# Kernel optimization log

Measured on AMD Instinct MI355X. Metric: run time of the kernel, lower is better.

## Reference

```python
import jax, jax.numpy as jnp
import numpy as np

N_LAYERS = 3

def setup_inputs() -> dict:
    key = jax.random.key(0)
    ks = jax.random.split(key, 16)
    N, E, F_in, H = 50000, 800000, 5, 64
    x = jax.random.normal(ks[0], (N, F_in), dtype=jnp.float32)
    edge_index = jax.random.randint(ks[1], (2, E), 0, N, dtype=jnp.int64)
    s = lambda fan_in: 1.0 / np.sqrt(fan_in)
    return {
        "x": x,
        "edge_index": edge_index,
        "W_enc": jax.random.uniform(ks[2], (F_in, H), jnp.float32, -s(F_in), s(F_in)),
        "b_enc": jnp.zeros((H,), jnp.float32),
        "conv_W": jax.random.uniform(ks[3], (N_LAYERS, H, H), jnp.float32, -s(H), s(H)),
        "conv_b": jnp.zeros((N_LAYERS, H), jnp.float32),
        "W_d1": jax.random.uniform(ks[4], (H, H // 2), jnp.float32, -s(H), s(H)),
        "b_d1": jnp.zeros((H // 2,), jnp.float32),
        "W_d2": jax.random.uniform(ks[5], (H // 2, 1), jnp.float32, -s(H // 2), s(H // 2)),
        "b_d2": jnp.zeros((1,), jnp.float32),
        "W_i1": jax.random.uniform(ks[6], (H, H // 2), jnp.float32, -s(H), s(H)),
        "b_i1": jnp.zeros((H // 2,), jnp.float32),
        "W_i2": jax.random.uniform(ks[7], (H // 2, 1), jnp.float32, -s(H // 2), s(H // 2)),
        "b_i2": jnp.zeros((1,), jnp.float32),
    }

def reference(x, edge_index, W_enc, b_enc, conv_W, conv_b,
              W_d1, b_d1, W_d2, b_d2, W_i1, b_i1, W_i2, b_i2):
    N = x.shape[0]
    # GCN normalization with self-loops (PyG GCNConv default):
    loops = jnp.arange(N, dtype=edge_index.dtype)
    row = jnp.concatenate([edge_index[0], loops])  # source
    col = jnp.concatenate([edge_index[1], loops])  # target
    deg = jax.ops.segment_sum(jnp.ones_like(row, dtype=x.dtype), col, num_segments=N)
    dinv = jax.lax.rsqrt(deg)  # deg >= 1 due to self-loops
    norm = dinv[row] * dinv[col]  # [E + N]

    h = jax.nn.relu(x @ W_enc + b_enc)  # [N, H]
    for l in range(N_LAYERS):
        hw = h @ conv_W[l]                       # [N, H]
        msg = hw[row] * norm[:, None]            # gather + scale
        agg = jax.ops.segment_sum(msg, col, num_segments=N)  # scatter-add
        h = jax.nn.relu(agg + conv_b[l])

    demand = jax.nn.relu(h @ W_d1 + b_d1) @ W_d2 + b_d2       # [N, 1]
    inventory = jax.nn.relu(h @ W_i1 + b_i1) @ W_i2 + b_i2    # [N, 1]
    return (demand, inventory)
```

## Files before the change

kernel.cpp:

```cpp
#include <hip/hip_runtime.h>
#include <hip/hip_bf16.h>


#define HDIM 64
#define PB 256
#define NPB 256
#define NPB_SHIFT 8

__device__ inline unsigned bfpack(float lo, float hi) {
    unsigned ul = __float_as_uint(lo), uh = __float_as_uint(hi);
    ul += 0x7fffu + ((ul >> 16) & 1u);
    uh += 0x7fffu + ((uh >> 16) & 1u);
    return (ul >> 16) | (uh & 0xffff0000u);
}

__device__ inline float2 bfunpack(unsigned u) {
    float2 r;
    r.x = __uint_as_float(u << 16);
    r.y = __uint_as_float(u & 0xffff0000u);
    return r;
}

__global__ __launch_bounds__(256) void hist_pass(const int* __restrict__ dst,
                                                 unsigned* __restrict__ histT,
                                                 int E, int NB) {
    __shared__ unsigned h[256];
    int t = threadIdx.x, p = blockIdx.x;
    h[t] = 0u;
    __syncthreads();
    int chunk = (E + PB - 1) / PB;
    int lo = p * chunk, hi = min(lo + chunk, E);
    for (int e = lo + t; e < hi; e += 256)
        atomicAdd(&h[dst[e] >> NPB_SHIFT], 1u);
    __syncthreads();
    if (t < NB) histT[t * PB + p] = h[t];
}

__global__ __launch_bounds__(PB) void scan_bucket(unsigned* __restrict__ histT,
                                                  unsigned* __restrict__ btot) {
    __shared__ unsigned s[PB];
    int t = threadIdx.x, k = blockIdx.x;
    unsigned v = histT[k * PB + t];
    s[t] = v;
    __syncthreads();
#pragma unroll
    for (int off = 1; off < PB; off <<= 1) {
        unsigned u = (t >= off) ? s[t - off] : 0u;
        __syncthreads();
        s[t] += u;
        __syncthreads();
    }
    histT[k * PB + t] = s[t] - v;
    if (t == PB - 1) btot[k] = s[t];
}

__global__ __launch_bounds__(256) void bin_pass(const int* __restrict__ ei,
                                                const unsigned* __restrict__ histT,
                                                const unsigned* __restrict__ btot,
                                                unsigned* __restrict__ ebuf,
                                                int E, int NB) {
    __shared__ unsigned bb[256];
    __shared__ unsigned cur[256];
    int t = threadIdx.x, p = blockIdx.x;
    unsigned bv = (t < NB) ? btot[t] : 0u;
    bb[t] = bv;
    __syncthreads();
#pragma unroll
    for (int off = 1; off < 256; off <<= 1) {
        unsigned u = (t >= off) ? bb[t - off] : 0u;
        __syncthreads();
        bb[t] += u;
        __syncthreads();
    }
    if (t < NB) cur[t] = histT[t * PB + p] + (bb[t] - bv);
    __syncthreads();
    int chunk = (E + PB - 1) / PB;
    int lo = p * chunk, hi = min(lo + chunk, E);
    for (int e = lo + t; e < hi; e += 256) {
        unsigned sN = (unsigned)ei[e];
        unsigned dN = (unsigned)ei[E + e];
        unsigned pos = atomicAdd(&cur[dN >> NPB_SHIFT], 1u);
        ebuf[pos] = ((dN & (NPB - 1u)) << 16) | sN;
    }
}

__global__ __launch_bounds__(256) void csr_pass(const unsigned* __restrict__ ebuf,
                                                const unsigned* __restrict__ btot,
                                                unsigned* __restrict__ row_ptr,
                                                float* __restrict__ dinv,
                                                int* __restrict__ csr_src,
                                                int N, int E, int NB) {
    __shared__ unsigned bb[256];
    __shared__ unsigned cntL[NPB];
    __shared__ unsigned sc[NPB];
    __shared__ unsigned cur[NPB];
    int t = threadIdx.x, k = blockIdx.x;
    unsigned bv = (t < NB) ? btot[t] : 0u;
    bb[t] = bv;
    __syncthreads();
#pragma unroll
    for (int off = 1; off < 256; off <<= 1) {
        unsigned u = (t >= off) ? bb[t - off] : 0u;
        __syncthreads();
        bb[t] += u;
        __syncthreads();
    }
    unsigned e1 = bb[k];
    unsigned e0 = e1 - btot[k];
    int nbase = k << NPB_SHIFT;
    cntL[t] = 0u;
    __syncthreads();
    for (unsigned e = e0 + t; e < e1; e += 256)
        atomicAdd(&cntL[ebuf[e] >> 16], 1u);
    __syncthreads();
    unsigned v = cntL[t];
    sc[t] = v;
    __syncthreads();
#pragma unroll
    for (int off = 1; off < NPB; off <<= 1) {
        unsigned u = (t >= off) ? sc[t - off] : 0u;
        __syncthreads();
        sc[t] += u;
        __syncthreads();
    }
    unsigned pos0 = e0 + sc[t] - v;
    cur[t] = pos0;
    int node = nbase + t;
    if (node < N) {
        row_ptr[node] = pos0;
        dinv[node] = rsqrtf((float)(v + 1u));
    }
    if (k == NB - 1 && t == 0) row_ptr[N] = (unsigned)E;
    __syncthreads();
    for (unsigned e = e0 + t; e < e1; e += 256) {
        unsigned ed = ebuf[e];
        unsigned pos = atomicAdd(&cur[ed >> 16], 1u);
        csr_src[pos] = (int)(ed & 0xffffu);
    }
}

__global__ __launch_bounds__(256) void encoder(const float* __restrict__ x,
                                               const float* __restrict__ W,
                                               const float* __restrict__ b,
                                               const float* __restrict__ dinv,
                                               unsigned* __restrict__ hn, int N) {
    int t = blockIdx.x * 256 + threadIdx.x;
    int i = t >> 5, jp = t & 31;
    if (i >= N) return;
    int j0 = 2 * jp;
    float a0 = b[j0], a1 = b[j0 + 1];
#pragma unroll
    for (int k = 0; k < 5; k++) {
        float xv = x[i * 5 + k];
        a0 = fmaf(xv, W[k * 64 + j0], a0);
        a1 = fmaf(xv, W[k * 64 + j0 + 1], a1);
    }
    float di = dinv[i];
    hn[t] = bfpack(di * fmaxf(a0, 0.0f), di * fmaxf(a1, 0.0f));
}

#define ACC4(A, V) do {                                                         \
    float2 _p = bfunpack((V).x), _q = bfunpack((V).y);                          \
    (A).x += _p.x; (A).y += _p.y; (A).z += _q.x; (A).w += _q.y;                 \
} while (0)

#define MACC4(A, V, C) do {                                                     \
    float2 _p = bfunpack((V).x), _q = bfunpack((V).y);                          \
    (A).x += (C) ? _p.x : 0.f; (A).y += (C) ? _p.y : 0.f;                       \
    (A).z += (C) ? _q.x : 0.f; (A).w += (C) ? _q.y : 0.f;                       \
} while (0)

__device__ inline float4 gather_row_q(const unsigned* __restrict__ row_ptr,
                                      const int* __restrict__ csr_src,
                                      const uint2* __restrict__ hp,
                                      int i, int fl) {
    uint2 sv = hp[(size_t)i * 16 + fl];
    float4 a0, a1 = {0.f, 0.f, 0.f, 0.f}, a2 = a1, a3 = a1;
    {
        float2 p = bfunpack(sv.x), q = bfunpack(sv.y);
        a0.x = p.x; a0.y = p.y; a0.z = q.x; a0.w = q.y;
    }
    unsigned e0 = row_ptr[i];
    unsigned cnt = row_ptr[i + 1] - e0;
    const int* idx = csr_src + e0;
    unsigned u = 0;
    if (cnt >= 8) {
        int s0 = idx[0], s1 = idx[1], s2 = idx[2], s3 = idx[3];
        int s4 = idx[4], s5 = idx[5], s6 = idx[6], s7 = idx[7];
        while (true) {
            uint2 v0 = hp[(size_t)s0 * 16 + fl];
            uint2 v1 = hp[(size_t)s1 * 16 + fl];
            uint2 v2 = hp[(size_t)s2 * 16 + fl];
            uint2 v3 = hp[(size_t)s3 * 16 + fl];
            uint2 v4 = hp[(size_t)s4 * 16 + fl];
            uint2 v5 = hp[(size_t)s5 * 16 + fl];
            uint2 v6 = hp[(size_t)s6 * 16 + fl];
            uint2 v7 = hp[(size_t)s7 * 16 + fl];
            unsigned un = u + 8;
            bool more = (un + 8 <= cnt);
            if (more) {
                s0 = idx[un + 0]; s1 = idx[un + 1]; s2 = idx[un + 2]; s3 = idx[un + 3];
                s4 = idx[un + 4]; s5 = idx[un + 5]; s6 = idx[un + 6]; s7 = idx[un + 7];
            }
            ACC4(a0, v0); ACC4(a1, v1); ACC4(a2, v2); ACC4(a3, v3);
            ACC4(a0, v4); ACC4(a1, v5); ACC4(a2, v6); ACC4(a3, v7);
            u = un;
            if (!more) break;
        }
    }
    if (u < cnt) {
        unsigned last = cnt - 1;
        int t0 = idx[u];
        int t1 = idx[min(u + 1, last)];
        int t2 = idx[min(u + 2, last)];
        int t3 = idx[min(u + 3, last)];
        int t4 = idx[min(u + 4, last)];
        int t5 = idx[min(u + 5, last)];
        int t6 = idx[min(u + 6, last)];
        int t7 = idx[min(u + 7, last)];
        uint2 w0 = hp[(size_t)t0 * 16 + fl];
        uint2 w1 = hp[(size_t)t1 * 16 + fl];
        uint2 w2 = hp[(size_t)t2 * 16 + fl];
        uint2 w3 = hp[(size_t)t3 * 16 + fl];
        uint2 w4 = hp[(size_t)t4 * 16 + fl];
        uint2 w5 = hp[(size_t)t5 * 16 + fl];
        uint2 w6 = hp[(size_t)t6 * 16 + fl];
        uint2 w7 = hp[(size_t)t7 * 16 + fl];
        ACC4(a0, w0);
        MACC4(a1, w1, u + 1 < cnt);
        MACC4(a2, w2, u + 2 < cnt);
        MACC4(a3, w3, u + 3 < cnt);
        MACC4(a0, w4, u + 4 < cnt);
        MACC4(a1, w5, u + 5 < cnt);
        MACC4(a2, w6, u + 6 < cnt);
        MACC4(a3, w7, u + 7 < cnt);
    }
    a0.x += a1.x; a0.y += a1.y; a0.z += a1.z; a0.w += a1.w;
    a2.x += a3.x; a2.y += a3.y; a2.z += a3.z; a2.w += a3.w;
    a0.x += a2.x; a0.y += a2.y; a0.z += a2.z; a0.w += a2.w;
    return a0;
}

#define CONV_K8(WROW, HK) do {                                                  \
    float4 wa = ((const float4*)(WROW))[0];                                     \
    float4 wb = ((const float4*)(WROW))[1];                                     \
    acc0.x = fmaf(HK, wa.x, acc0.x); acc0.y = fmaf(HK, wa.y, acc0.y);           \
    acc0.z = fmaf(HK, wa.z, acc0.z); acc0.w = fmaf(HK, wa.w, acc0.w);           \
    acc1.x = fmaf(HK, wb.x, acc1.x); acc1.y = fmaf(HK, wb.y, acc1.y);           \
    acc1.z = fmaf(HK, wb.z, acc1.z); acc1.w = fmaf(HK, wb.w, acc1.w);           \
} while (0)

__global__ __launch_bounds__(512, 6) void gconv(const unsigned* __restrict__ row_ptr,
                                                const int* __restrict__ csr_src,
                                                const unsigned* __restrict__ hn_in,
                                                const float* __restrict__ W,
                                                const float* __restrict__ b,
                                                const float* __restrict__ dinv,
                                                unsigned* __restrict__ hn_out, int N) {
    __shared__ float ybuf[64 * 65];
    int tid = threadIdx.x;
    int qw = tid >> 4, fl = tid & 15;
    int base = blockIdx.x * 64;
    for (int s = 0; s < 2; s++) {
        int n = qw * 2 + s;
        int i = base + n;
        if (i < N) {
            float4 a = gather_row_q(row_ptr, csr_src, (const uint2*)hn_in, i, fl);
            ybuf[(4 * fl + 0) * 65 + n] = a.x;
            ybuf[(4 * fl + 1) * 65 + n] = a.y;
            ybuf[(4 * fl + 2) * 65 + n] = a.z;
            ybuf[(4 * fl + 3) * 65 + n] = a.w;
        }
    }
    __syncthreads();
    int n = tid & 63;
    int qt = __builtin_amdgcn_readfirstlane(tid >> 6);
    int i = base + n;
    if (i >= N) return;
    int jb = qt * 8;
    float di = dinv[i];
    float4 acc0 = {0.f, 0.f, 0.f, 0.f}, acc1 = acc0;
    const float* Wj = W + jb;
#pragma unroll
    for (int k = 0; k < 64; k++) {
        float hk = ybuf[k * 65 + n];
        CONV_K8(Wj + k * 64, hk);
    }
    const float* bj = b + jb;
    float4 y0, y1;
    y0.x = fmaxf(fmaf(di, acc0.x, bj[0]), 0.f) * di;
    y0.y = fmaxf(fmaf(di, acc0.y, bj[1]), 0.f) * di;
    y0.z = fmaxf(fmaf(di, acc0.z, bj[2]), 0.f) * di;
    y0.w = fmaxf(fmaf(di, acc0.w, bj[3]), 0.f) * di;
    y1.x = fmaxf(fmaf(di, acc1.x, bj[4]), 0.f) * di;
    y1.y = fmaxf(fmaf(di, acc1.y, bj[5]), 0.f) * di;
    y1.z = fmaxf(fmaf(di, acc1.z, bj[6]), 0.f) * di;
    y1.w = fmaxf(fmaf(di, acc1.w, bj[7]), 0.f) * di;
    uint4 p;
    p.x = bfpack(y0.x, y0.y);
    p.y = bfpack(y0.z, y0.w);
    p.z = bfpack(y1.x, y1.y);
    p.w = bfpack(y1.z, y1.w);
    *(uint4*)(hn_out + (size_t)i * 32 + qt * 4) = p;
}

__global__ __launch_bounds__(512, 6) void gconv_heads(const unsigned* __restrict__ row_ptr,
                                                      const int* __restrict__ csr_src,
                                                      const unsigned* __restrict__ hn_in,
                                                      const float* __restrict__ W,
                                                      const float* __restrict__ b,
                                                      const float* __restrict__ dinv,
                                                      const float* __restrict__ W_d1, const float* __restrict__ b_d1,
                                                      const float* __restrict__ W_d2, const float* __restrict__ b_d2,
                                                      const float* __restrict__ W_i1, const float* __restrict__ b_i1,
                                                      const float* __restrict__ W_i2, const float* __restrict__ b_i2,
                                                      float* __restrict__ out, int N) {
    __shared__ float ybuf[64 * 65];
    __shared__ float opart[512];
    int tid = threadIdx.x;
    int qw = tid >> 4, fl = tid & 15;
    int base = blockIdx.x * 64;
    for (int s = 0; s < 2; s++) {
        int n = qw * 2 + s;
        int i = base + n;
        if (i < N) {
            float4 a = gather_row_q(row_ptr, csr_src, (const uint2*)hn_in, i, fl);
            ybuf[(4 * fl + 0) * 65 + n] = a.x;
            ybuf[(4 * fl + 1) * 65 + n] = a.y;
            ybuf[(4 * fl + 2) * 65 + n] = a.z;
            ybuf[(4 * fl + 3) * 65 + n] = a.w;
        }
    }
    __syncthreads();
    int n = tid & 63;
    int qt = __builtin_amdgcn_readfirstlane(tid >> 6);
    int i = base + n;
    int jb = qt * 8;
    float y[8];
    if (i < N) {
        float di = dinv[i];
        float4 acc0 = {0.f, 0.f, 0.f, 0.f}, acc1 = acc0;
        const float* Wj = W + jb;
#pragma unroll
        for (int k = 0; k < 64; k++) {
            float hk = ybuf[k * 65 + n];
            CONV_K8(Wj + k * 64, hk);
        }
        const float* bj = b + jb;
        y[0] = fmaxf(fmaf(di, acc0.x, bj[0]), 0.f);
        y[1] = fmaxf(fmaf(di, acc0.y, bj[1]), 0.f);
        y[2] = fmaxf(fmaf(di, acc0.z, bj[2]), 0.f);
        y[3] = fmaxf(fmaf(di, acc0.w, bj[3]), 0.f);
        y[4] = fmaxf(fmaf(di, acc1.x, bj[4]), 0.f);
        y[5] = fmaxf(fmaf(di, acc1.y, bj[5]), 0.f);
        y[6] = fmaxf(fmaf(di, acc1.z, bj[6]), 0.f);
        y[7] = fmaxf(fmaf(di, acc1.w, bj[7]), 0.f);
    }
    __syncthreads();
    if (i < N) {
#pragma unroll
        for (int jj = 0; jj < 8; jj++) ybuf[(jb + jj) * 65 + n] = y[jj];
    }
    __syncthreads();
    int hd = __builtin_amdgcn_readfirstlane(tid >> 8);
    int q2 = __builtin_amdgcn_readfirstlane((tid >> 6) & 3);
    int hb = q2 * 8;
    float op = 0.f;
    if (i < N) {
        const float* W1 = (hd ? W_i1 : W_d1) + hb;
        const float* b1 = (hd ? b_i1 : b_d1) + hb;
        const float* W2 = (hd ? W_i2 : W_d2) + hb;
        float4 acc0 = {0.f, 0.f, 0.f, 0.f}, acc1 = acc0;
#pragma unroll
        for (int k = 0; k < 64; k++) {
            float hk = ybuf[k * 65 + n];
            CONV_K8(W1 + k * 32, hk);
        }
        op = fmaf(fmaxf(acc0.x + b1[0], 0.f), W2[0], op);
        op = fmaf(fmaxf(acc0.y + b1[1], 0.f), W2[1], op);
        op = fmaf(fmaxf(acc0.z + b1[2], 0.f), W2[2], op);
        op = fmaf(fmaxf(acc0.w + b1[3], 0.f), W2[3], op);
        op = fmaf(fmaxf(acc1.x + b1[4], 0.f), W2[4], op);
        op = fmaf(fmaxf(acc1.y + b1[5], 0.f), W2[5], op);
        op = fmaf(fmaxf(acc1.z + b1[6], 0.f), W2[6], op);
        op = fmaf(fmaxf(acc1.w + b1[7], 0.f), W2[7], op);
    }
    opart[tid] = op;
    __syncthreads();
    if (tid < 128) {
        int n2 = tid & 63, h2 = tid >> 6;
        int i2 = base + n2;
        if (i2 < N) {
            int o0 = h2 * 256 + n2;
            float o = opart[o0] + opart[o0 + 64] + opart[o0 + 128] + opart[o0 + 192]
                    + (h2 ? b_i2[0] : b_d2[0]);
            out[(size_t)h2 * N + i2] = o;
        }
    }
}

extern "C" void kernel_launch(void* const* d_in, const int* in_sizes, int n_in,
                              void* d_out, int out_size, void* d_ws, size_t ws_size,
                              hipStream_t stream) {
    const float* x      = (const float*)d_in[0];
    const int*   ei     = (const int*)d_in[1];
    const float* W_enc  = (const float*)d_in[2];
    const float* b_enc  = (const float*)d_in[3];
    const float* conv_W = (const float*)d_in[4];
    const float* conv_b = (const float*)d_in[5];
    const float* W_d1   = (const float*)d_in[6];
    const float* b_d1   = (const float*)d_in[7];
    const float* W_d2   = (const float*)d_in[8];
    const float* b_d2   = (const float*)d_in[9];
    const float* W_i1   = (const float*)d_in[10];
    const float* b_i1   = (const float*)d_in[11];
    const float* W_i2   = (const float*)d_in[12];
    const float* b_i2   = (const float*)d_in[13];

    const int N = in_sizes[0] / 5;
    const int E = in_sizes[1] / 2;
    const int NB = (N + NPB - 1) >> NPB_SHIFT;

    float* g    = (float*)d_ws;
    unsigned* hnA = (unsigned*)d_ws;
    unsigned* hnB = (unsigned*)(g + (size_t)N * HDIM);
    float* dinv = (float*)(hnB + (size_t)N * 32);
    unsigned* row_ptr = (unsigned*)(dinv + N);
    unsigned* histT   = row_ptr + N + 1;
    unsigned* btot    = histT + (size_t)NB * PB;
    int* csr_src      = (int*)(btot + NB);
    unsigned* ebuf    = (unsigned*)d_ws;
    float* out = (float*)d_out;

    const int gBlocks = (N + 63) / 64;

    hist_pass<<<PB, 256, 0, stream>>>(ei + E, histT, E, NB);
    scan_bucket<<<NB, PB, 0, stream>>>(histT, btot);
    bin_pass<<<PB, 256, 0, stream>>>(ei, histT, btot, ebuf, E, NB);
    csr_pass<<<NB, 256, 0, stream>>>(ebuf, btot, row_ptr, dinv, csr_src, N, E, NB);

    encoder<<<(N * 32 + 255) / 256, 256, 0, stream>>>(x, W_enc, b_enc, dinv, hnA, N);

    gconv<<<gBlocks, 512, 0, stream>>>(row_ptr, csr_src, hnA,
                                       conv_W + 0 * HDIM * HDIM, conv_b + 0 * HDIM,
                                       dinv, hnB, N);
    gconv<<<gBlocks, 512, 0, stream>>>(row_ptr, csr_src, hnB,
                                       conv_W + 1 * HDIM * HDIM, conv_b + 1 * HDIM,
                                       dinv, hnA, N);
    gconv_heads<<<gBlocks, 512, 0, stream>>>(row_ptr, csr_src, hnA,
                                             conv_W + 2 * HDIM * HDIM, conv_b + 2 * HDIM,
                                             dinv, W_d1, b_d1, W_d2, b_d2,
                                             W_i1, b_i1, W_i2, b_i2, out, N);
}
```

Measured before the change: 223.2 us.

## Split neighbor gather by source half into two passes for cache locality

Partitions each node's CSR neighbor list by whether the source index is below a fixed midpoint (NHALF). Each layer then runs two kernels: a first pass gathers from the low half and writes fp32 partial sums to a scratch buffer, and a second pass gathers from the high half, adds the partial, and does the dense transform. The aim is to keep each pass's randomly gathered working set small enough to stay resident in cache. The cost is an extra kernel launch per layer plus writing and reading a fp32 N×64 partial buffer. Nontemporal loads and stores are used so this streaming traffic does not evict the gathered data.

Measured after the change: 263.2 us. 17.9% more time.

```diff
diff --git a/kernel.cpp b/kernel.cpp
--- a/kernel.cpp
+++ b/kernel.cpp
@@ -6,6 +6,7 @@
 #define PB 256
 #define NPB 256
 #define NPB_SHIFT 8
+#define NHALF 25000
 
 __device__ inline unsigned bfpack(float lo, float hi) {
     unsigned ul = __float_as_uint(lo), uh = __float_as_uint(hi);
@@ -19,6 +20,27 @@
     r.x = __uint_as_float(u << 16);
     r.y = __uint_as_float(u & 0xffff0000u);
     return r;
+}
+
+__device__ inline void nt_store4(float* p, float4 v) {
+    __builtin_nontemporal_store(v.x, p + 0);
+    __builtin_nontemporal_store(v.y, p + 1);
+    __builtin_nontemporal_store(v.z, p + 2);
+    __builtin_nontemporal_store(v.w, p + 3);
+}
+__device__ inline float4 nt_load4(const float* p) {
+    float4 v;
+    v.x = __builtin_nontemporal_load(p + 0);
+    v.y = __builtin_nontemporal_load(p + 1);
+    v.z = __builtin_nontemporal_load(p + 2);
+    v.w = __builtin_nontemporal_load(p + 3);
+    return v;
+}
+__device__ inline void nt_store4u(unsigned* p, uint4 v) {
+    __builtin_nontemporal_store(v.x, p + 0);
+    __builtin_nontemporal_store(v.y, p + 1);
+    __builtin_nontemporal_store(v.z, p + 2);
+    __builtin_nontemporal_store(v.w, p + 3);
 }
 
 __global__ __launch_bounds__(256) void hist_pass(const int* __restrict__ dst,
@@ -87,13 +109,16 @@
 __global__ __launch_bounds__(256) void csr_pass(const unsigned* __restrict__ ebuf,
                                                 const unsigned* __restrict__ btot,
                                                 unsigned* __restrict__ row_ptr,
+                                                unsigned* __restrict__ midp,
                                                 float* __restrict__ dinv,
                                                 int* __restrict__ csr_src,
                                                 int N, int E, int NB) {
     __shared__ unsigned bb[256];
     __shared__ unsigned cntL[NPB];
+    __shared__ unsigned cnt0[NPB];
     __shared__ unsigned sc[NPB];
-    __shared__ unsigned cur[NPB];
+    __shared__ unsigned curA[NPB];
+    __shared__ unsigned curB[NPB];
     int t = threadIdx.x, k = blockIdx.x;
     unsigned bv = (t < NB) ? btot[t] : 0u;
     bb[t] = bv;
@@ -109,9 +134,14 @@
     unsigned e0 = e1 - btot[k];
     int nbase = k << NPB_SHIFT;
     cntL[t] = 0u;
-    __syncthreads();
-    for (unsigned e = e0 + t; e < e1; e += 256)
-        atomicAdd(&cntL[ebuf[e] >> 16], 1u);
+    cnt0[t] = 0u;
+    __syncthreads();
+    for (unsigned e = e0 + t; e < e1; e += 256) {
+        unsigned ed = ebuf[e];
+        unsigned local = ed >> 16;
+        atomicAdd(&cntL[local], 1u);
+        if ((ed & 0xffffu) < NHALF) atomicAdd(&cnt0[local], 1u);
+    }
     __syncthreads();
     unsigned v = cntL[t];
     sc[t] = v;
@@ -124,18 +154,23 @@
         __syncthreads();
     }
     unsigned pos0 = e0 + sc[t] - v;
-    cur[t] = pos0;
+    curA[t] = pos0;
+    curB[t] = pos0 + cnt0[t];
     int node = nbase + t;
     if (node < N) {
         row_ptr[node] = pos0;
+        midp[node] = pos0 + cnt0[t];
         dinv[node] = rsqrtf((float)(v + 1u));
     }
     if (k == NB - 1 && t == 0) row_ptr[N] = (unsigned)E;
     __syncthreads();
     for (unsigned e = e0 + t; e < e1; e += 256) {
         unsigned ed = ebuf[e];
-        unsigned pos = atomicAdd(&cur[ed >> 16], 1u);
-        csr_src[pos] = (int)(ed & 0xffffu);
+        unsigned local = ed >> 16;
+        unsigned src = ed & 0xffffu;
+        unsigned pos = (src < NHALF) ? atomicAdd(&curA[local], 1u)
+                                     : atomicAdd(&curB[local], 1u);
+        csr_src[pos] = (int)src;
     }
 }
 
@@ -170,19 +205,10 @@
     (A).z += (C) ? _q.x : 0.f; (A).w += (C) ? _q.y : 0.f;                       \
 } while (0)
 
-__device__ inline float4 gather_row_q(const unsigned* __restrict__ row_ptr,
-                                      const int* __restrict__ csr_src,
-                                      const uint2* __restrict__ hp,
-                                      int i, int fl) {
-    uint2 sv = hp[(size_t)i * 16 + fl];
-    float4 a0, a1 = {0.f, 0.f, 0.f, 0.f}, a2 = a1, a3 = a1;
-    {
-        float2 p = bfunpack(sv.x), q = bfunpack(sv.y);
-        a0.x = p.x; a0.y = p.y; a0.z = q.x; a0.w = q.y;
-    }
-    unsigned e0 = row_ptr[i];
-    unsigned cnt = row_ptr[i + 1] - e0;
-    const int* idx = csr_src + e0;
+__device__ inline float4 gather_range_q(const int* __restrict__ idx, unsigned cnt,
+                                        const uint2* __restrict__ hp, int fl,
+                                        float4 a0) {
+    float4 a1 = {0.f, 0.f, 0.f, 0.f}, a2 = a1, a3 = a1;
     unsigned u = 0;
     if (cnt >= 8) {
         int s0 = idx[0], s1 = idx[1], s2 = idx[2], s3 = idx[3];
@@ -241,6 +267,33 @@
     return a0;
 }
 
+__global__ __launch_bounds__(512, 6) void gpart(const unsigned* __restrict__ row_ptr,
+                                                const unsigned* __restrict__ midp,
+                                                const int* __restrict__ csr_src,
+                                                const unsigned* __restrict__ hn_in,
+                                                float* __restrict__ g, int N) {
+    int tid = threadIdx.x;
+    int qw = tid >> 4, fl = tid & 15;
+    int base = blockIdx.x * 64;
+    const uint2* hp = (const uint2*)hn_in;
+    for (int s = 0; s < 2; s++) {
+        int n = qw * 2 + s;
+        int i = base + n;
+        if (i < N) {
+            unsigned e0 = row_ptr[i];
+            unsigned e1 = midp[i];
+            float4 a = {0.f, 0.f, 0.f, 0.f};
+            if (i < NHALF) {
+                uint2 sv = hp[(size_t)i * 16 + fl];
+                float2 p = bfunpack(sv.x), q = bfunpack(sv.y);
+                a.x = p.x; a.y = p.y; a.z = q.x; a.w = q.y;
+            }
+            a = gather_range_q(csr_src + e0, e1 - e0, hp, fl, a);
+            nt_store4(g + (size_t)i * 64 + 4 * fl, a);
+        }
+    }
+}
+
 #define CONV_K8(WROW, HK) do {                                                  \
     float4 wa = ((const float4*)(WROW))[0];                                     \
     float4 wb = ((const float4*)(WROW))[1];                                     \
@@ -250,22 +303,35 @@
     acc1.z = fmaf(HK, wb.z, acc1.z); acc1.w = fmaf(HK, wb.w, acc1.w);           \
 } while (0)
 
-__global__ __launch_bounds__(512, 6) void gconv(const unsigned* __restrict__ row_ptr,
-                                                const int* __restrict__ csr_src,
-                                                const unsigned* __restrict__ hn_in,
-                                                const float* __restrict__ W,
-                                                const float* __restrict__ b,
-                                                const float* __restrict__ dinv,
-                                                unsigned* __restrict__ hn_out, int N) {
+__global__ __launch_bounds__(512, 6) void gconvB(const unsigned* __restrict__ row_ptr,
+                                                 const unsigned* __restrict__ midp,
+                                                 const int* __restrict__ csr_src,
+                                                 const unsigned* __restrict__ hn_in,
+                                                 const float* __restrict__ g,
+                                                 const float* __restrict__ W,
+                                                 const float* __restrict__ b,
+                                                 const float* __restrict__ dinv,
+                                                 unsigned* __restrict__ hn_out, int N) {
     __shared__ float ybuf[64 * 65];
     int tid = threadIdx.x;
     int qw = tid >> 4, fl = tid & 15;
     int base = blockIdx.x * 64;
+    const uint2* hp = (const uint2*)hn_in;
     for (int s = 0; s < 2; s++) {
         int n = qw * 2 + s;
         int i = base + n;
         if (i < N) {
-            float4 a = gather_row_q(row_ptr, csr_src, (const uint2*)hn_in, i, fl);
+            unsigned e0 = midp[i];
+            unsigned e1 = row_ptr[i + 1];
+            float4 a = {0.f, 0.f, 0.f, 0.f};
+            if (i >= NHALF) {
+                uint2 sv = hp[(size_t)i * 16 + fl];
+                float2 p = bfunpack(sv.x), q = bfunpack(sv.y);
+                a.x = p.x; a.y = p.y; a.z = q.x; a.w = q.y;
+            }
+            a = gather_range_q(csr_src + e0, e1 - e0, hp, fl, a);
+            float4 part = nt_load4(g + (size_t)i * 64 + 4 * fl);
+            a.x += part.x; a.y += part.y; a.z += part.z; a.w += part.w;
             ybuf[(4 * fl + 0) * 65 + n] = a.x;
             ybuf[(4 * fl + 1) * 65 + n] = a.y;
             ybuf[(4 * fl + 2) * 65 + n] = a.z;
@@ -301,30 +367,43 @@
     p.y = bfpack(y0.z, y0.w);
     p.z = bfpack(y1.x, y1.y);
     p.w = bfpack(y1.z, y1.w);
-    *(uint4*)(hn_out + (size_t)i * 32 + qt * 4) = p;
-}
-
-__global__ __launch_bounds__(512, 6) void gconv_heads(const unsigned* __restrict__ row_ptr,
-                                                      const int* __restrict__ csr_src,
-                                                      const unsigned* __restrict__ hn_in,
-                                                      const float* __restrict__ W,
-                                                      const float* __restrict__ b,
-                                                      const float* __restrict__ dinv,
-                                                      const float* __restrict__ W_d1, const float* __restrict__ b_d1,
-                                                      const float* __restrict__ W_d2, const float* __restrict__ b_d2,
-                                                      const float* __restrict__ W_i1, const float* __restrict__ b_i1,
-                                                      const float* __restrict__ W_i2, const float* __restrict__ b_i2,
-                                                      float* __restrict__ out, int N) {
+    nt_store4u(hn_out + (size_t)i * 32 + qt * 4, p);
+}
+
+__global__ __launch_bounds__(512, 6) void gconvB_heads(const unsigned* __restrict__ row_ptr,
+                                                       const unsigned* __restrict__ midp,
+                                                       const int* __restrict__ csr_src,
+                                                       const unsigned* __restrict__ hn_in,
+                                                       const float* __restrict__ g,
+                                                       const float* __restrict__ W,
+                                                       const float* __restrict__ b,
+                                                       const float* __restrict__ dinv,
+                                                       const float* __restrict__ W_d1, const float* __restrict__ b_d1,
+                                                       const float* __restrict__ W_d2, const float* __restrict__ b_d2,
+                                                       const float* __restrict__ W_i1, const float* __restrict__ b_i1,
+                                                       const float* __restrict__ W_i2, const float* __restrict__ b_i2,
+                                                       float* __restrict__ out, int N) {
     __shared__ float ybuf[64 * 65];
     __shared__ float opart[512];
     int tid = threadIdx.x;
     int qw = tid >> 4, fl = tid & 15;
     int base = blockIdx.x * 64;
+    const uint2* hp = (const uint2*)hn_in;
     for (int s = 0; s < 2; s++) {
         int n = qw * 2 + s;
         int i = base + n;
         if (i < N) {
-            float4 a = gather_row_q(row_ptr, csr_src, (const uint2*)hn_in, i, fl);
+            unsigned e0 = midp[i];
+            unsigned e1 = row_ptr[i + 1];
+            float4 a = {0.f, 0.f, 0.f, 0.f};
+            if (i >= NHALF) {
+                uint2 sv = hp[(size_t)i * 16 + fl];
+                float2 p = bfunpack(sv.x), q = bfunpack(sv.y);
+                a.x = p.x; a.y = p.y; a.z = q.x; a.w = q.y;
+            }
+            a = gather_range_q(csr_src + e0, e1 - e0, hp, fl, a);
+            float4 part = nt_load4(g + (size_t)i * 64 + 4 * fl);
+            a.x += part.x; a.y += part.y; a.z += part.z; a.w += part.w;
             ybuf[(4 * fl + 0) * 65 + n] = a.x;
             ybuf[(4 * fl + 1) * 65 + n] = a.y;
             ybuf[(4 * fl + 2) * 65 + n] = a.z;
@@ -422,11 +501,12 @@
     const int NB = (N + NPB - 1) >> NPB_SHIFT;
 
     float* g    = (float*)d_ws;
-    unsigned* hnA = (unsigned*)d_ws;
-    unsigned* hnB = (unsigned*)(g + (size_t)N * HDIM);
+    unsigned* hnA = (unsigned*)(g + (size_t)N * HDIM);
+    unsigned* hnB = hnA + (size_t)N * 32;
     float* dinv = (float*)(hnB + (size_t)N * 32);
     unsigned* row_ptr = (unsigned*)(dinv + N);
-    unsigned* histT   = row_ptr + N + 1;
+    unsigned* midp    = row_ptr + N + 1;
+    unsigned* histT   = midp + N;
     unsigned* btot    = histT + (size_t)NB * PB;
     int* csr_src      = (int*)(btot + NB);
     unsigned* ebuf    = (unsigned*)d_ws;
@@ -437,18 +517,21 @@
     hist_pass<<<PB, 256, 0, stream>>>(ei + E, histT, E, NB);
     scan_bucket<<<NB, PB, 0, stream>>>(histT, btot);
     bin_pass<<<PB, 256, 0, stream>>>(ei, histT, btot, ebuf, E, NB);
-    csr_pass<<<NB, 256, 0, stream>>>(ebuf, btot, row_ptr, dinv, csr_src, N, E, NB);
+    csr_pass<<<NB, 256, 0, stream>>>(ebuf, btot, row_ptr, midp, dinv, csr_src, N, E, NB);
 
     encoder<<<(N * 32 + 255) / 256, 256, 0, stream>>>(x, W_enc, b_enc, dinv, hnA, N);
 
-    gconv<<<gBlocks, 512, 0, stream>>>(row_ptr, csr_src, hnA,
-                                       conv_W + 0 * HDIM * HDIM, conv_b + 0 * HDIM,
-                                       dinv, hnB, N);
-    gconv<<<gBlocks, 512, 0, stream>>>(row_ptr, csr_src, hnB,
-                                       conv_W + 1 * HDIM * HDIM, conv_b + 1 * HDIM,
-                                       dinv, hnA, N);
-    gconv_heads<<<gBlocks, 512, 0, stream>>>(row_ptr, csr_src, hnA,
-                                             conv_W + 2 * HDIM * HDIM, conv_b + 2 * HDIM,
-                                             dinv, W_d1, b_d1, W_d2, b_d2,
-                                             W_i1, b_i1, W_i2, b_i2, out, N);
-}
+    gpart<<<gBlocks, 512, 0, stream>>>(row_ptr, midp, csr_src, hnA, g, N);
+    gconvB<<<gBlocks, 512, 0, stream>>>(row_ptr, midp, csr_src, hnA, g,
+                                        conv_W + 0 * HDIM * HDIM, conv_b + 0 * HDIM,
+                                        dinv, hnB, N);
+    gpart<<<gBlocks, 512, 0, stream>>>(row_ptr, midp, csr_src, hnB, g, N);
+    gconvB<<<gBlocks, 512, 0, stream>>>(row_ptr, midp, csr_src, hnB, g,
+                                        conv_W + 1 * HDIM * HDIM, conv_b + 1 * HDIM,
+                                        dinv, hnA, N);
+    gpart<<<gBlocks, 512, 0, stream>>>(row_ptr, midp, csr_src, hnA, g, N);
+    gconvB_heads<<<gBlocks, 512, 0, stream>>>(row_ptr, midp, csr_src, hnA, g,
+                                              conv_W + 2 * HDIM * HDIM, conv_b + 2 * HDIM,
+                                              dinv, W_d1, b_d1, W_d2, b_d2,
+                                              W_i1, b_i1, W_i2, b_i2, out, N);
+}
```

## Pad CSR neighbor lists to multiples of eight with a zero sentinel row

Applied to the files above, without the earlier changes.

Each node's neighbor list is padded to a multiple of 8 inside fixed-capacity per-bucket slabs, with pad entries pointing at an extra zero feature row N. The gather loop then drops its masked tail iteration and the row_ptr[i+1] read, and uses a per-node count of 8-blocks stored as uint16. Padding adds wasted gathers of the zero row (on average about 3.5 per node). The fixed BCAP=8192 slab per bucket assumes no bucket holds more than that many padded edges. Launch bounds occupancy hint is lowered from 6 to 4.

Measured after the change: 207.2 us (median of 2 runs). 1.08x faster.

```diff
diff --git a/kernel.cpp b/kernel.cpp
--- a/kernel.cpp
+++ b/kernel.cpp
@@ -6,6 +6,7 @@
 #define PB 256
 #define NPB 256
 #define NPB_SHIFT 8
+#define BCAP 8192
 
 __device__ inline unsigned bfpack(float lo, float hi) {
     unsigned ul = __float_as_uint(lo), uh = __float_as_uint(hi);
@@ -87,8 +88,9 @@
 __global__ __launch_bounds__(256) void csr_pass(const unsigned* __restrict__ ebuf,
                                                 const unsigned* __restrict__ btot,
                                                 unsigned* __restrict__ row_ptr,
+                                                unsigned short* __restrict__ pc8,
                                                 float* __restrict__ dinv,
-                                                int* __restrict__ csr_src,
+                                                int* __restrict__ csr_pad,
                                                 int N, int E, int NB) {
     __shared__ unsigned bb[256];
     __shared__ unsigned cntL[NPB];
@@ -114,7 +116,8 @@
         atomicAdd(&cntL[ebuf[e] >> 16], 1u);
     __syncthreads();
     unsigned v = cntL[t];
-    sc[t] = v;
+    unsigned pcnt = (v + 7u) & ~7u;
+    sc[t] = pcnt;
     __syncthreads();
 #pragma unroll
     for (int off = 1; off < NPB; off <<= 1) {
@@ -123,19 +126,20 @@
         sc[t] += u;
         __syncthreads();
     }
-    unsigned pos0 = e0 + sc[t] - v;
+    unsigned pos0 = (unsigned)k * BCAP + (sc[t] - pcnt);
     cur[t] = pos0;
     int node = nbase + t;
     if (node < N) {
         row_ptr[node] = pos0;
+        pc8[node] = (unsigned short)(pcnt >> 3);
         dinv[node] = rsqrtf((float)(v + 1u));
-    }
-    if (k == NB - 1 && t == 0) row_ptr[N] = (unsigned)E;
+        for (unsigned j = v; j < pcnt; j++) csr_pad[pos0 + j] = N;
+    }
     __syncthreads();
     for (unsigned e = e0 + t; e < e1; e += 256) {
         unsigned ed = ebuf[e];
         unsigned pos = atomicAdd(&cur[ed >> 16], 1u);
-        csr_src[pos] = (int)(ed & 0xffffu);
+        csr_pad[pos] = (int)(ed & 0xffffu);
     }
 }
 
@@ -143,10 +147,16 @@
                                                const float* __restrict__ W,
                                                const float* __restrict__ b,
                                                const float* __restrict__ dinv,
-                                               unsigned* __restrict__ hn, int N) {
+                                               unsigned* __restrict__ hnA,
+                                               unsigned* __restrict__ hnB, int N) {
     int t = blockIdx.x * 256 + threadIdx.x;
     int i = t >> 5, jp = t & 31;
-    if (i >= N) return;
+    if (i > N) return;
+    if (i == N) {
+        hnA[t] = 0u;
+        hnB[t] = 0u;
+        return;
+    }
     int j0 = 2 * jp;
     float a0 = b[j0], a1 = b[j0 + 1];
 #pragma unroll
@@ -156,7 +166,7 @@
         a1 = fmaf(xv, W[k * 64 + j0 + 1], a1);
     }
     float di = dinv[i];
-    hn[t] = bfpack(di * fmaxf(a0, 0.0f), di * fmaxf(a1, 0.0f));
+    hnA[t] = bfpack(di * fmaxf(a0, 0.0f), di * fmaxf(a1, 0.0f));
 }
 
 #define ACC4(A, V) do {                                                         \
@@ -164,29 +174,14 @@
     (A).x += _p.x; (A).y += _p.y; (A).z += _q.x; (A).w += _q.y;                 \
 } while (0)
 
-#define MACC4(A, V, C) do {                                                     \
-    float2 _p = bfunpack((V).x), _q = bfunpack((V).y);                          \
-    (A).x += (C) ? _p.x : 0.f; (A).y += (C) ? _p.y : 0.f;                       \
-    (A).z += (C) ? _q.x : 0.f; (A).w += (C) ? _q.y : 0.f;                       \
-} while (0)
-
-__device__ inline float4 gather_row_q(const unsigned* __restrict__ row_ptr,
-                                      const int* __restrict__ csr_src,
-                                      const uint2* __restrict__ hp,
-                                      int i, int fl) {
-    uint2 sv = hp[(size_t)i * 16 + fl];
-    float4 a0, a1 = {0.f, 0.f, 0.f, 0.f}, a2 = a1, a3 = a1;
-    {
-        float2 p = bfunpack(sv.x), q = bfunpack(sv.y);
-        a0.x = p.x; a0.y = p.y; a0.z = q.x; a0.w = q.y;
-    }
-    unsigned e0 = row_ptr[i];
-    unsigned cnt = row_ptr[i + 1] - e0;
-    const int* idx = csr_src + e0;
-    unsigned u = 0;
-    if (cnt >= 8) {
+__device__ inline float4 gather_pad_q(const int* __restrict__ idx, int nb,
+                                      const uint2* __restrict__ hp, int fl,
+                                      float4 a0) {
+    float4 a1 = {0.f, 0.f, 0.f, 0.f}, a2 = a1, a3 = a1;
+    if (nb > 0) {
         int s0 = idx[0], s1 = idx[1], s2 = idx[2], s3 = idx[3];
         int s4 = idx[4], s5 = idx[5], s6 = idx[6], s7 = idx[7];
+        int u = 0;
         while (true) {
             uint2 v0 = hp[(size_t)s0 * 16 + fl];
             uint2 v1 = hp[(size_t)s1 * 16 + fl];
@@ -196,44 +191,16 @@
             uint2 v5 = hp[(size_t)s5 * 16 + fl];
             uint2 v6 = hp[(size_t)s6 * 16 + fl];
             uint2 v7 = hp[(size_t)s7 * 16 + fl];
-            unsigned un = u + 8;
-            bool more = (un + 8 <= cnt);
+            u += 8;
+            bool more = (u >> 3) < nb;
             if (more) {
-                s0 = idx[un + 0]; s1 = idx[un + 1]; s2 = idx[un + 2]; s3 = idx[un + 3];
-                s4 = idx[un + 4]; s5 = idx[un + 5]; s6 = idx[un + 6]; s7 = idx[un + 7];
+                s0 = idx[u + 0]; s1 = idx[u + 1]; s2 = idx[u + 2]; s3 = idx[u + 3];
+                s4 = idx[u + 4]; s5 = idx[u + 5]; s6 = idx[u + 6]; s7 = idx[u + 7];
             }
             ACC4(a0, v0); ACC4(a1, v1); ACC4(a2, v2); ACC4(a3, v3);
             ACC4(a0, v4); ACC4(a1, v5); ACC4(a2, v6); ACC4(a3, v7);
-            u = un;
             if (!more) break;
         }
-    }
-    if (u < cnt) {
-        unsigned last = cnt - 1;
-        int t0 = idx[u];
-        int t1 = idx[min(u + 1, last)];
-        int t2 = idx[min(u + 2, last)];
-        int t3 = idx[min(u + 3, last)];
-        int t4 = idx[min(u + 4, last)];
-        int t5 = idx[min(u + 5, last)];
-        int t6 = idx[min(u + 6, last)];
-        int t7 = idx[min(u + 7, last)];
-        uint2 w0 = hp[(size_t)t0 * 16 + fl];
-        uint2 w1 = hp[(size_t)t1 * 16 + fl];
-        uint2 w2 = hp[(size_t)t2 * 16 + fl];
-        uint2 w3 = hp[(size_t)t3 * 16 + fl];
-        uint2 w4 = hp[(size_t)t4 * 16 + fl];
-        uint2 w5 = hp[(size_t)t5 * 16 + fl];
-        uint2 w6 = hp[(size_t)t6 * 16 + fl];
-        uint2 w7 = hp[(size_t)t7 * 16 + fl];
-        ACC4(a0, w0);
-        MACC4(a1, w1, u + 1 < cnt);
-        MACC4(a2, w2, u + 2 < cnt);
-        MACC4(a3, w3, u + 3 < cnt);
-        MACC4(a0, w4, u + 4 < cnt);
-        MACC4(a1, w5, u + 5 < cnt);
-        MACC4(a2, w6, u + 6 < cnt);
-        MACC4(a3, w7, u + 7 < cnt);
     }
     a0.x += a1.x; a0.y += a1.y; a0.z += a1.z; a0.w += a1.w;
     a2.x += a3.x; a2.y += a3.y; a2.z += a3.z; a2.w += a3.w;
@@ -250,8 +217,9 @@
     acc1.z = fmaf(HK, wb.z, acc1.z); acc1.w = fmaf(HK, wb.w, acc1.w);           \
 } while (0)
 
-__global__ __launch_bounds__(512, 6) void gconv(const unsigned* __restrict__ row_ptr,
-                                                const int* __restrict__ csr_src,
+__global__ __launch_bounds__(512, 4) void gconv(const unsigned* __restrict__ row_ptr,
+                                                const unsigned short* __restrict__ pc8,
+                                                const int* __restrict__ csr_pad,
                                                 const unsigned* __restrict__ hn_in,
                                                 const float* __restrict__ W,
                                                 const float* __restrict__ b,
@@ -261,11 +229,16 @@
     int tid = threadIdx.x;
     int qw = tid >> 4, fl = tid & 15;
     int base = blockIdx.x * 64;
+    const uint2* hp = (const uint2*)hn_in;
     for (int s = 0; s < 2; s++) {
         int n = qw * 2 + s;
         int i = base + n;
         if (i < N) {
-            float4 a = gather_row_q(row_ptr, csr_src, (const uint2*)hn_in, i, fl);
+            uint2 sv = hp[(size_t)i * 16 + fl];
+            float4 a;
+            float2 p = bfunpack(sv.x), q = bfunpack(sv.y);
+            a.x = p.x; a.y = p.y; a.z = q.x; a.w = q.y;
+            a = gather_pad_q(csr_pad + row_ptr[i], (int)pc8[i], hp, fl, a);
             ybuf[(4 * fl + 0) * 65 + n] = a.x;
             ybuf[(4 * fl + 1) * 65 + n] = a.y;
             ybuf[(4 * fl + 2) * 65 + n] = a.z;
@@ -304,8 +277,9 @@
     *(uint4*)(hn_out + (size_t)i * 32 + qt * 4) = p;
 }
 
-__global__ __launch_bounds__(512, 6) void gconv_heads(const unsigned* __restrict__ row_ptr,
-                                                      const int* __restrict__ csr_src,
+__global__ __launch_bounds__(512, 4) void gconv_heads(const unsigned* __restrict__ row_ptr,
+                                                      const unsigned short* __restrict__ pc8,
+                                                      const int* __restrict__ csr_pad,
                                                       const unsigned* __restrict__ hn_in,
                                                       const float* __restrict__ W,
                                                       const float* __restrict__ b,
@@ -320,11 +294,16 @@
     int tid = threadIdx.x;
     int qw = tid >> 4, fl = tid & 15;
     int base = blockIdx.x * 64;
+    const uint2* hp = (const uint2*)hn_in;
     for (int s = 0; s < 2; s++) {
         int n = qw * 2 + s;
         int i = base + n;
         if (i < N) {
-            float4 a = gather_row_q(row_ptr, csr_src, (const uint2*)hn_in, i, fl);
+            uint2 sv = hp[(size_t)i * 16 + fl];
+            float4 a;
+            float2 p = bfunpack(sv.x), q = bfunpack(sv.y);
+            a.x = p.x; a.y = p.y; a.z = q.x; a.w = q.y;
+            a = gather_pad_q(csr_pad + row_ptr[i], (int)pc8[i], hp, fl, a);
             ybuf[(4 * fl + 0) * 65 + n] = a.x;
             ybuf[(4 * fl + 1) * 65 + n] = a.y;
             ybuf[(4 * fl + 2) * 65 + n] = a.z;
@@ -421,15 +400,15 @@
     const int E = in_sizes[1] / 2;
     const int NB = (N + NPB - 1) >> NPB_SHIFT;
 
-    float* g    = (float*)d_ws;
     unsigned* hnA = (unsigned*)d_ws;
-    unsigned* hnB = (unsigned*)(g + (size_t)N * HDIM);
-    float* dinv = (float*)(hnB + (size_t)N * 32);
+    unsigned* hnB = hnA + (size_t)(N + 1) * 32;
+    float* dinv = (float*)(hnB + (size_t)(N + 1) * 32);
     unsigned* row_ptr = (unsigned*)(dinv + N);
-    unsigned* histT   = row_ptr + N + 1;
-    unsigned* btot    = histT + (size_t)NB * PB;
-    int* csr_src      = (int*)(btot + NB);
-    unsigned* ebuf    = (unsigned*)d_ws;
+    unsigned short* pc8 = (unsigned short*)(row_ptr + N);
+    unsigned* histT = (unsigned*)(pc8 + N);
+    unsigned* btot  = histT + (size_t)NB * PB;
+    int* csr_pad    = (int*)(btot + NB);
+    unsigned* ebuf  = (unsigned*)d_ws;
     float* out = (float*)d_out;
 
     const int gBlocks = (N + 63) / 64;
@@ -437,17 +416,18 @@
     hist_pass<<<PB, 256, 0, stream>>>(ei + E, histT, E, NB);
     scan_bucket<<<NB, PB, 0, stream>>>(histT, btot);
     bin_pass<<<PB, 256, 0, stream>>>(ei, histT, btot, ebuf, E, NB);
-    csr_pass<<<NB, 256, 0, stream>>>(ebuf, btot, row_ptr, dinv, csr_src, N, E, NB);
-
-    encoder<<<(N * 32 + 255) / 256, 256, 0, stream>>>(x, W_enc, b_enc, dinv, hnA, N);
-
-    gconv<<<gBlocks, 512, 0, stream>>>(row_ptr, csr_src, hnA,
+    csr_pass<<<NB, 256, 0, stream>>>(ebuf, btot, row_ptr, pc8, dinv, csr_pad, N, E, NB);
+
+    encoder<<<((N + 1) * 32 + 255) / 256, 256, 0, stream>>>(x, W_enc, b_enc, dinv,
+                                                            hnA, hnB, N);
+
+    gconv<<<gBlocks, 512, 0, stream>>>(row_ptr, pc8, csr_pad, hnA,
                                        conv_W + 0 * HDIM * HDIM, conv_b + 0 * HDIM,
                                        dinv, hnB, N);
-    gconv<<<gBlocks, 512, 0, stream>>>(row_ptr, csr_src, hnB,
+    gconv<<<gBlocks, 512, 0, stream>>>(row_ptr, pc8, csr_pad, hnB,
                                        conv_W + 1 * HDIM * HDIM, conv_b + 1 * HDIM,
                                        dinv, hnA, N);
-    gconv_heads<<<gBlocks, 512, 0, stream>>>(row_ptr, csr_src, hnA,
+    gconv_heads<<<gBlocks, 512, 0, stream>>>(row_ptr, pc8, csr_pad, hnA,
                                              conv_W + 2 * HDIM * HDIM, conv_b + 2 * HDIM,
                                              dinv, W_d1, b_d1, W_d2, b_d2,
                                              W_i1, b_i1, W_i2, b_i2, out, N);
```
